# Optimization experiments

Measured on AMD Instinct MI355X. Metric: run time of the kernel, lower is better.

Reference implementation:

```python
import jax, jax.numpy as jnp
import numpy as np

B, L, D, H = 2, 1024, 1024, 16
HD = D // H  # head_dim = 64
EPS = 1e-12  # F.normalize default eps


def setup_inputs() -> dict:
    key = jax.random.key(0)
    ks = jax.random.split(key, 7)
    s = 1.0 / np.sqrt(D)
    return {
        "x": jax.random.normal(ks[0], (B, L, D), dtype=jnp.float32),
        "Wq": jax.random.normal(ks[1], (D, D), dtype=jnp.float32) * s,
        "Wk": jax.random.normal(ks[2], (D, D), dtype=jnp.float32) * s,
        "Wv": jax.random.normal(ks[3], (D, D), dtype=jnp.float32) * s,
        "Wo": jax.random.normal(ks[4], (D, D), dtype=jnp.float32) * s,
        "Wb": jax.random.normal(ks[5], (D, H), dtype=jnp.float32) * s,
        "bb": jnp.zeros((H,), dtype=jnp.float32),
    }


def _l2norm(t):
    # matches F.normalize(t, dim=-1): t / max(||t||_2, eps)
    n = jnp.sqrt(jnp.sum(t * t, axis=-1, keepdims=True))
    return t / jnp.maximum(n, EPS)


def reference(x, Wq, Wk, Wv, Wo, Wb, bb):
    q = (x @ Wq).reshape(B, L, H, HD)
    k = (x @ Wk).reshape(B, L, H, HD)
    v = (x @ Wv).reshape(B, L, H, HD)
    beta = jax.nn.sigmoid(x @ Wb + bb)          # [B, L, H]
    q = _l2norm(q)
    k = _l2norm(k)
    # gated outer products: [B, L, H, HD, HD]
    kv = jnp.einsum('blhd,blhe->blhde', k, v) * beta[..., None, None]
    kv_cumsum = jnp.cumsum(kv, axis=1)          # causal cumulative kv state
    out = jnp.einsum('blhd,blhde->blhe', q, kv_cumsum)  # [B, L, H, HD]
    return out.reshape(B, L, D) @ Wo
```

## Files before the change

kernel.cpp:

```cpp
#include <hip/hip_runtime.h>
#include <math.h>

#define BB   2
#define LL   1024
#define DD   1024
#define HH   16
#define HDIM 64
#define MM   (BB * LL)
#define CHK  64
#define NCHK (LL / CHK)

typedef short bf16x8 __attribute__((ext_vector_type(8)));
typedef float f32x4  __attribute__((ext_vector_type(4)));
typedef const __attribute__((address_space(1))) unsigned int* gas_ptr;
typedef __attribute__((address_space(3))) unsigned int* las_ptr;

__device__ __forceinline__ void gload16(const void* g, void* l) {
    __builtin_amdgcn_global_load_lds((gas_ptr)(unsigned long long)g,
                                     (las_ptr)(unsigned long long)l, 16, 0, 0);
}

__device__ __forceinline__ unsigned short f2bf(float f) {
    unsigned int u = __float_as_uint(f);
    u += 0x7fffu + ((u >> 16) & 1u);
    return (unsigned short)(u >> 16);
}
__device__ __forceinline__ float bfhi(unsigned int u) { return __uint_as_float(u & 0xffff0000u); }
__device__ __forceinline__ float bflo(unsigned int u) { return __uint_as_float(u << 16); }

__device__ __forceinline__ bf16x8 frag70(const unsigned short* a, int row, int tc) {
    const unsigned int* p = (const unsigned int*)(a + row * 70 + tc);
    union { unsigned int u[4]; bf16x8 v; } r;
    r.u[0] = p[0]; r.u[1] = p[1]; r.u[2] = p[2]; r.u[3] = p[3];
    return r.v;
}

__global__ void prep_kernel(const float* __restrict__ x, unsigned short* __restrict__ xb,
                            const float* __restrict__ Wb, float* __restrict__ Wbt) {
    const int bid = blockIdx.x;
    if (bid < 2048) {
        const int idx = bid * 256 + threadIdx.x;
        const float4 v = ((const float4*)x)[idx];
        ushort4 o;
        o.x = f2bf(v.x); o.y = f2bf(v.y); o.z = f2bf(v.z); o.w = f2bf(v.w);
        ((ushort4*)xb)[idx] = o;
    } else {
        const int t = (bid - 2048) * 256 + threadIdx.x;
        const int h = t >> 10, k = t & 1023;
        Wbt[t] = Wb[k * HH + h];
    }
}

__global__ void transpose_cast(const float* __restrict__ W0, const float* __restrict__ W1,
                               const float* __restrict__ W2, const float* __restrict__ W3,
                               unsigned short* __restrict__ T0, unsigned short* __restrict__ T1,
                               unsigned short* __restrict__ T2, unsigned short* __restrict__ T3) {
    __shared__ float tile[32][33];
    const int which = blockIdx.x >> 10;
    const int b = blockIdx.x & 1023;
    const int bk = b >> 5, bn = b & 31;
    const float* W = which == 0 ? W0 : which == 1 ? W1 : which == 2 ? W2 : W3;
    unsigned short* T = which == 0 ? T0 : which == 1 ? T1 : which == 2 ? T2 : T3;
    const int tx = threadIdx.x & 31, ty = threadIdx.x >> 5;
#pragma unroll
    for (int i = 0; i < 4; ++i)
        tile[ty + i * 8][tx] = W[(size_t)(bk * 32 + ty + i * 8) * DD + bn * 32 + tx];
    __syncthreads();
#pragma unroll
    for (int i = 0; i < 4; ++i)
        T[(size_t)(bn * 32 + ty + i * 8) * DD + bk * 32 + tx] = f2bf(tile[tx][ty + i * 8]);
}

__device__ __forceinline__ void gemm_kloop(const unsigned short* A, const unsigned short* Bt,
                                           unsigned short* As, unsigned short* Bs,
                                           int rowBase, int colBase, int K,
                                           f32x4 acc[4][4]) {
    const int tid = threadIdx.x;
    const int c0 = tid, c1 = tid + 256;
    const int ar0 = c0 >> 2, ak0 = (c0 & 3) << 3;
    const int ar1 = c1 >> 2, ak1 = (c1 & 3) << 3;
    const unsigned short* Ag0 = A + (size_t)(rowBase + ar0) * K + ak0;
    const unsigned short* Ag1 = A + (size_t)(rowBase + ar1) * K + ak1;
    const unsigned short* Bg0 = Bt + (size_t)(colBase + ar0) * K + ak0;
    const unsigned short* Bg1 = Bt + (size_t)(colBase + ar1) * K + ak1;
    unsigned short* Al0 = As + c0 * 8; unsigned short* Al1 = As + c1 * 8;
    unsigned short* Bl0 = Bs + c0 * 8; unsigned short* Bl1 = Bs + c1 * 8;
    const int lane = tid & 63, wv = tid >> 6;
    const int qr = wv >> 1, qc = wv & 1;
    const int fr = lane & 15;
    const int koff = (lane >> 4) << 3;
    int aoff[4], boff[4];
#pragma unroll
    for (int mi = 0; mi < 4; ++mi) aoff[mi] = (qr * 64 + mi * 16 + fr) * 32 + koff;
#pragma unroll
    for (int nj = 0; nj < 4; ++nj) boff[nj] = (qc * 64 + nj * 16 + fr) * 32 + koff;

    for (int k0 = 0; k0 < K; k0 += 32) {
        __syncthreads();
        gload16(Ag0, Al0); gload16(Ag1, Al1);
        gload16(Bg0, Bl0); gload16(Bg1, Bl1);
        Ag0 += 32; Ag1 += 32; Bg0 += 32; Bg1 += 32;
        __syncthreads();
        bf16x8 av[4], bv[4];
#pragma unroll
        for (int mi = 0; mi < 4; ++mi) av[mi] = *(const bf16x8*)(As + aoff[mi]);
#pragma unroll
        for (int nj = 0; nj < 4; ++nj) bv[nj] = *(const bf16x8*)(Bs + boff[nj]);
#pragma unroll
        for (int mi = 0; mi < 4; ++mi)
#pragma unroll
            for (int nj = 0; nj < 4; ++nj)
                acc[mi][nj] = __builtin_amdgcn_mfma_f32_16x16x32_bf16(av[mi], bv[nj], acc[mi][nj], 0, 0, 0);
    }
}

__global__ __launch_bounds__(256) void gemm_qkv(const unsigned short* __restrict__ xb,
                                                const unsigned short* __restrict__ Wqt,
                                                const unsigned short* __restrict__ Wkt,
                                                const unsigned short* __restrict__ Wvt,
                                                unsigned short* __restrict__ qb,
                                                unsigned short* __restrict__ kb,
                                                unsigned short* __restrict__ vb) {
    __shared__ unsigned short As[128 * 32];
    __shared__ unsigned short Bs[128 * 32];
    const int by = blockIdx.x / 24, bxx = blockIdx.x % 24;
    const int mat = bxx >> 3, tn = bxx & 7;
    const unsigned short* Bt = mat == 0 ? Wqt : (mat == 1 ? Wkt : Wvt);
    unsigned short* Cout = mat == 0 ? qb : (mat == 1 ? kb : vb);
    f32x4 acc[4][4];
#pragma unroll
    for (int mi = 0; mi < 4; ++mi)
#pragma unroll
        for (int nj = 0; nj < 4; ++nj) acc[mi][nj] = (f32x4){0.f, 0.f, 0.f, 0.f};
    gemm_kloop(xb, Bt, As, Bs, by * 128, tn * 128, DD, acc);

    const int lane = threadIdx.x & 63, wv = threadIdx.x >> 6;
    const int qr = wv >> 1, qc = wv & 1;
    if (mat < 2) {
#pragma unroll
        for (int mi = 0; mi < 4; ++mi)
#pragma unroll
            for (int i = 0; i < 4; ++i) {
                float s = 0.f;
#pragma unroll
                for (int nj = 0; nj < 4; ++nj) { float t = acc[mi][nj][i]; s += t * t; }
                s += __shfl_xor(s, 1, 64);
                s += __shfl_xor(s, 2, 64);
                s += __shfl_xor(s, 4, 64);
                s += __shfl_xor(s, 8, 64);
                const float inv = 1.0f / fmaxf(sqrtf(s), 1e-12f);
#pragma unroll
                for (int nj = 0; nj < 4; ++nj) acc[mi][nj][i] *= inv;
            }
    }
#pragma unroll
    for (int mi = 0; mi < 4; ++mi)
#pragma unroll
        for (int i = 0; i < 4; ++i) {
            const int row = by * 128 + qr * 64 + mi * 16 + (lane >> 4) * 4 + i;
#pragma unroll
            for (int nj = 0; nj < 4; ++nj) {
                const int col = tn * 128 + qc * 64 + nj * 16 + (lane & 15);
                Cout[(size_t)row * DD + col] = f2bf(acc[mi][nj][i]);
            }
        }
}

__global__ __launch_bounds__(256) void gemm_out(const unsigned short* __restrict__ yb,
                                                const unsigned short* __restrict__ Wot,
                                                float* __restrict__ out) {
    __shared__ unsigned short As[64 * 32];
    __shared__ unsigned short Bs[128 * 32];
    const int by = blockIdx.x >> 3, tn = blockIdx.x & 7;
    const int tid = threadIdx.x;
    const int rowBase = by * 64, colBase = tn * 128;
    const int ar = tid >> 2, ak = (tid & 3) << 3;
    const unsigned short* Ag = yb + (size_t)(rowBase + ar) * DD + ak;
    unsigned short* Al = As + tid * 8;
    const int c1 = tid + 256;
    const int br1 = c1 >> 2, bk1 = (c1 & 3) << 3;
    const unsigned short* Bg0 = Wot + (size_t)(colBase + ar) * DD + ak;
    const unsigned short* Bg1 = Wot + (size_t)(colBase + br1) * DD + bk1;
    unsigned short* Bl0 = Bs + tid * 8; unsigned short* Bl1 = Bs + c1 * 8;
    const int lane = tid & 63, wv = tid >> 6;
    const int rh = wv & 1, ch = wv >> 1;
    const int fr = lane & 15, koff = (lane >> 4) << 3;
    int aoff[2], boff[4];
#pragma unroll
    for (int mi = 0; mi < 2; ++mi) aoff[mi] = (rh * 32 + mi * 16 + fr) * 32 + koff;
#pragma unroll
    for (int nj = 0; nj < 4; ++nj) boff[nj] = (ch * 64 + nj * 16 + fr) * 32 + koff;
    f32x4 acc[2][4];
#pragma unroll
    for (int mi = 0; mi < 2; ++mi)
#pragma unroll
        for (int nj = 0; nj < 4; ++nj) acc[mi][nj] = (f32x4){0.f, 0.f, 0.f, 0.f};
    for (int k0 = 0; k0 < DD; k0 += 32) {
        __syncthreads();
        gload16(Ag, Al); gload16(Bg0, Bl0); gload16(Bg1, Bl1);
        Ag += 32; Bg0 += 32; Bg1 += 32;
        __syncthreads();
        bf16x8 av[2], bv[4];
#pragma unroll
        for (int mi = 0; mi < 2; ++mi) av[mi] = *(const bf16x8*)(As + aoff[mi]);
#pragma unroll
        for (int nj = 0; nj < 4; ++nj) bv[nj] = *(const bf16x8*)(Bs + boff[nj]);
#pragma unroll
        for (int mi = 0; mi < 2; ++mi)
#pragma unroll
            for (int nj = 0; nj < 4; ++nj)
                acc[mi][nj] = __builtin_amdgcn_mfma_f32_16x16x32_bf16(av[mi], bv[nj], acc[mi][nj], 0, 0, 0);
    }
    const int quad = lane >> 4;
#pragma unroll
    for (int mi = 0; mi < 2; ++mi)
#pragma unroll
        for (int i = 0; i < 4; ++i) {
            const int row = rowBase + rh * 32 + mi * 16 + quad * 4 + i;
#pragma unroll
            for (int nj = 0; nj < 4; ++nj) {
                const int col = colBase + ch * 64 + nj * 16 + fr;
                out[(size_t)row * DD + col] = acc[mi][nj][i];
            }
        }
}

__global__ void beta_kernel(const float* __restrict__ x, const float* __restrict__ Wbt,
                            const float* __restrict__ bias, float* __restrict__ beta) {
    const int m = blockIdx.x * 4 + (threadIdx.x >> 6);
    const int lane = threadIdx.x & 63;
    const float4* xr = (const float4*)(x + (size_t)m * DD);
    float4 xv[4];
#pragma unroll
    for (int i = 0; i < 4; ++i) xv[i] = xr[lane * 4 + i];
    float res = 0.f;
#pragma unroll
    for (int h = 0; h < HH; ++h) {
        const float4* wr = (const float4*)(Wbt + (size_t)h * DD);
        float s = 0.f;
#pragma unroll
        for (int i = 0; i < 4; ++i) {
            const float4 w = wr[lane * 4 + i];
            s += xv[i].x * w.x + xv[i].y * w.y + xv[i].z * w.z + xv[i].w * w.w;
        }
        s += __shfl_xor(s, 1, 64);  s += __shfl_xor(s, 2, 64);
        s += __shfl_xor(s, 4, 64);  s += __shfl_xor(s, 8, 64);
        s += __shfl_xor(s, 16, 64); s += __shfl_xor(s, 32, 64);
        if (lane == h) res = s;
    }
    if (lane < HH) beta[m * HH + lane] = 1.0f / (1.0f + expf(-(res + bias[lane])));
}

__global__ __launch_bounds__(256) void chunkkv_kernel(const unsigned short* __restrict__ k,
                                                      const unsigned short* __restrict__ v,
                                                      const float* __restrict__ beta,
                                                      float* __restrict__ states) {
    const int c = blockIdx.x % NCHK;
    const int bh = blockIdx.x / NCHK;
    const int b = bh / HH, h = bh % HH;
    __shared__ unsigned short kT[64 * 70];
    __shared__ unsigned short vT[64 * 70];
    const int tid = threadIdx.x;
    for (int i = tid; i < 512; i += 256) {
        const int t = i >> 3, dg = (i & 7) << 3;
        const int m = b * LL + c * CHK + t;
        const float be = beta[m * HH + h];
        const size_t go = (size_t)m * DD + h * 64 + dg;
        const uint4 ku = *(const uint4*)&k[go];
        const uint4 vu = *(const uint4*)&v[go];
        unsigned int kw[4] = {ku.x, ku.y, ku.z, ku.w};
        unsigned int vw[4] = {vu.x, vu.y, vu.z, vu.w};
#pragma unroll
        for (int jj = 0; jj < 4; ++jj) {
            kT[(dg + 2 * jj)     * 70 + t] = f2bf(bflo(kw[jj]) * be);
            kT[(dg + 2 * jj + 1) * 70 + t] = f2bf(bfhi(kw[jj]) * be);
            vT[(dg + 2 * jj)     * 70 + t] = (unsigned short)(vw[jj] & 0xffffu);
            vT[(dg + 2 * jj + 1) * 70 + t] = (unsigned short)(vw[jj] >> 16);
        }
    }
    __syncthreads();
    const int lane = tid & 63, wv = tid >> 6;
    const int fr = lane & 15, quad = lane >> 4;
    f32x4 acc[4];
#pragma unroll
    for (int et = 0; et < 4; ++et) acc[et] = (f32x4){0.f, 0.f, 0.f, 0.f};
#pragma unroll
    for (int kh = 0; kh < 2; ++kh) {
        const int tc = kh * 32 + quad * 8;
        const bf16x8 a = frag70(kT, wv * 16 + fr, tc);
#pragma unroll
        for (int et = 0; et < 4; ++et) {
            const bf16x8 bb = frag70(vT, et * 16 + fr, tc);
            acc[et] = __builtin_amdgcn_mfma_f32_16x16x32_bf16(a, bb, acc[et], 0, 0, 0);
        }
    }
    float* outp = states + ((size_t)bh * NCHK + c) * 4096;
#pragma unroll
    for (int et = 0; et < 4; ++et)
#pragma unroll
        for (int i = 0; i < 4; ++i) {
            const int d = wv * 16 + quad * 4 + i;
            const int e = et * 16 + fr;
            outp[d * 64 + e] = acc[et][i];
        }
}

__global__ void prefix_kernel(float* __restrict__ states) {
    const int bh = blockIdx.x >> 4, pg = blockIdx.x & 15;
    float* base = states + (size_t)bh * NCHK * 4096 + pg * 256 + threadIdx.x;
    float vals[NCHK];
#pragma unroll
    for (int c = 0; c < NCHK; ++c) vals[c] = base[c * 4096];
    float run = 0.0f;
#pragma unroll
    for (int c = 0; c < NCHK; ++c) {
        base[c * 4096] = run;
        run += vals[c];
    }
}

__global__ __launch_bounds__(256) void attn_kernel(const unsigned short* __restrict__ q,
                                                   const unsigned short* __restrict__ k,
                                                   const unsigned short* __restrict__ v,
                                                   const float* __restrict__ beta,
                                                   const float* __restrict__ states,
                                                   unsigned short* __restrict__ y) {
    const int c = blockIdx.x % NCHK;
    const int bh = blockIdx.x / NCHK;
    const int b = bh / HH, h = bh % HH;
    __shared__ unsigned short qS[64 * 80];
    __shared__ unsigned short kS[64 * 80];
    __shared__ unsigned short sS[64 * 80];
    __shared__ unsigned short vT[64 * 70];
    __shared__ unsigned short sT[64 * 70];
    const int tid = threadIdx.x;
    const float* stg = states + ((size_t)bh * NCHK + c) * 4096;
    for (int i = tid; i < 512; i += 256) {
        const int t = i >> 3, dg = (i & 7) << 3;
        const int m = b * LL + c * CHK + t;
        const float be = beta[m * HH + h];
        const size_t go = (size_t)m * DD + h * 64 + dg;
        const uint4 qu = *(const uint4*)&q[go];
        const uint4 ku = *(const uint4*)&k[go];
        const uint4 vu = *(const uint4*)&v[go];
        *(uint4*)&qS[t * 80 + dg] = qu;
        *(uint4*)&kS[t * 80 + dg] = ku;
        unsigned int vw[4] = {vu.x, vu.y, vu.z, vu.w};
#pragma unroll
        for (int jj = 0; jj < 4; ++jj) {
            vT[(dg + 2 * jj)     * 70 + t] = f2bf(bflo(vw[jj]) * be);
            vT[(dg + 2 * jj + 1) * 70 + t] = f2bf(bfhi(vw[jj]) * be);
        }
    }
    for (int i = tid; i < 1024; i += 256) {
        const int d = i >> 4, eg = (i & 15) << 2;
        const float4 s4 = ((const float4*)stg)[i];
        sT[(eg + 0) * 70 + d] = f2bf(s4.x);
        sT[(eg + 1) * 70 + d] = f2bf(s4.y);
        sT[(eg + 2) * 70 + d] = f2bf(s4.z);
        sT[(eg + 3) * 70 + d] = f2bf(s4.w);
    }
    __syncthreads();
    const int lane = tid & 63, wv = tid >> 6;
    const int fr = lane & 15, quad = lane >> 4;
    const int koff = quad * 8;
    f32x4 s_acc[4];
#pragma unroll
    for (int j = 0; j < 4; ++j) s_acc[j] = (f32x4){0.f, 0.f, 0.f, 0.f};
#pragma unroll
    for (int kh = 0; kh < 2; ++kh) {
        const bf16x8 a = *(const bf16x8*)&qS[(wv * 16 + fr) * 80 + kh * 32 + koff];
#pragma unroll
        for (int j = 0; j < 4; ++j) {
            const bf16x8 bb = *(const bf16x8*)&kS[(j * 16 + fr) * 80 + kh * 32 + koff];
            s_acc[j] = __builtin_amdgcn_mfma_f32_16x16x32_bf16(a, bb, s_acc[j], 0, 0, 0);
        }
    }
#pragma unroll
    for (int j = 0; j < 4; ++j)
#pragma unroll
        for (int i = 0; i < 4; ++i) {
            const int t = wv * 16 + quad * 4 + i;
            const int s = j * 16 + fr;
            sS[t * 80 + s] = (s <= t) ? f2bf(s_acc[j][i]) : (unsigned short)0;
        }
    f32x4 o_acc[4];
#pragma unroll
    for (int j = 0; j < 4; ++j) o_acc[j] = (f32x4){0.f, 0.f, 0.f, 0.f};
#pragma unroll
    for (int kh = 0; kh < 2; ++kh) {
        const bf16x8 a = *(const bf16x8*)&sS[(wv * 16 + fr) * 80 + kh * 32 + koff];
#pragma unroll
        for (int j = 0; j < 4; ++j) {
            const bf16x8 bb = frag70(vT, j * 16 + fr, kh * 32 + koff);
            o_acc[j] = __builtin_amdgcn_mfma_f32_16x16x32_bf16(a, bb, o_acc[j], 0, 0, 0);
        }
    }
#pragma unroll
    for (int kh = 0; kh < 2; ++kh) {
        const bf16x8 a = *(const bf16x8*)&qS[(wv * 16 + fr) * 80 + kh * 32 + koff];
#pragma unroll
        for (int j = 0; j < 4; ++j) {
            const bf16x8 bb = frag70(sT, j * 16 + fr, kh * 32 + koff);
            o_acc[j] = __builtin_amdgcn_mfma_f32_16x16x32_bf16(a, bb, o_acc[j], 0, 0, 0);
        }
    }
#pragma unroll
    for (int j = 0; j < 4; ++j)
#pragma unroll
        for (int i = 0; i < 4; ++i) {
            const int m = b * LL + c * CHK + wv * 16 + quad * 4 + i;
            const int e = j * 16 + fr;
            y[(size_t)m * DD + h * 64 + e] = f2bf(o_acc[j][i]);
        }
}

extern "C" void kernel_launch(void* const* d_in, const int* in_sizes, int n_in,
                              void* d_out, int out_size, void* d_ws, size_t ws_size,
                              hipStream_t stream) {
    (void)in_sizes; (void)n_in; (void)out_size; (void)ws_size;
    const float* x  = (const float*)d_in[0];
    const float* Wq = (const float*)d_in[1];
    const float* Wk = (const float*)d_in[2];
    const float* Wv = (const float*)d_in[3];
    const float* Wo = (const float*)d_in[4];
    const float* Wb = (const float*)d_in[5];
    const float* bbp = (const float*)d_in[6];
    float* out = (float*)d_out;

    char* ws = (char*)d_ws;
    unsigned short* xb  = (unsigned short*)ws;                      ws += (size_t)MM * DD * 2;
    unsigned short* Wqt = (unsigned short*)ws;                      ws += (size_t)DD * DD * 2;
    unsigned short* Wkt = (unsigned short*)ws;                      ws += (size_t)DD * DD * 2;
    unsigned short* Wvt = (unsigned short*)ws;                      ws += (size_t)DD * DD * 2;
    unsigned short* Wot = (unsigned short*)ws;                      ws += (size_t)DD * DD * 2;
    float*          Wbt = (float*)ws;                               ws += (size_t)HH * DD * 4;
    unsigned short* qb  = (unsigned short*)ws;                      ws += (size_t)MM * DD * 2;
    unsigned short* kb  = (unsigned short*)ws;                      ws += (size_t)MM * DD * 2;
    unsigned short* vb  = (unsigned short*)ws;                      ws += (size_t)MM * DD * 2;
    unsigned short* yb  = (unsigned short*)ws;                      ws += (size_t)MM * DD * 2;
    float*          beta   = (float*)ws;                            ws += (size_t)MM * HH * 4;
    float*          states = (float*)ws;                            ws += (size_t)BB * HH * NCHK * 4096 * 4;

    prep_kernel<<<2112, 256, 0, stream>>>(x, xb, Wb, Wbt);
    transpose_cast<<<4096, 256, 0, stream>>>(Wq, Wk, Wv, Wo, Wqt, Wkt, Wvt, Wot);
    gemm_qkv<<<16 * 24, 256, 0, stream>>>(xb, Wqt, Wkt, Wvt, qb, kb, vb);
    beta_kernel<<<MM / 4, 256, 0, stream>>>(x, Wbt, bbp, beta);
    chunkkv_kernel<<<BB * HH * NCHK, 256, 0, stream>>>(kb, vb, beta, states);
    prefix_kernel<<<BB * HH * NCHK, 256, 0, stream>>>(states);
    attn_kernel<<<BB * HH * NCHK, 256, 0, stream>>>(qb, kb, vb, beta, states, yb);
    gemm_out<<<32 * 8, 256, 0, stream>>>(yb, Wot, out);
}
```

Baseline: 155.3 us.

## Fuse prep kernels, compute beta via MFMA in QKV GEMM, sequential chunk scan

Merges the input-cast and weight-transpose kernels into one launch, moves the beta projection into extra blocks of the QKV GEMM using bf16 MFMA, and replaces the three-kernel chunked state pipeline (chunk kv, prefix, attention) with one scan kernel per batch-head. The scan keeps the running state in registers, so the global state buffer and two launches go away. The cost is that the scan runs only 32 blocks, each walking 16 chunks serially, which leaves most CUs idle. Beta now uses bf16 inputs, which lowers its precision.

```diff
diff --git a/kernel.cpp b/kernel.cpp
--- a/kernel.cpp
+++ b/kernel.cpp
@@ -35,8 +35,12 @@
     return r.v;
 }
 
-__global__ void prep_kernel(const float* __restrict__ x, unsigned short* __restrict__ xb,
-                            const float* __restrict__ Wb, float* __restrict__ Wbt) {
+__global__ void prep_all(const float* __restrict__ x, unsigned short* __restrict__ xb,
+                         const float* __restrict__ Wb, unsigned short* __restrict__ Wbt,
+                         const float* __restrict__ W0, const float* __restrict__ W1,
+                         const float* __restrict__ W2, const float* __restrict__ W3,
+                         unsigned short* __restrict__ T0, unsigned short* __restrict__ T1,
+                         unsigned short* __restrict__ T2, unsigned short* __restrict__ T3) {
     const int bid = blockIdx.x;
     if (bid < 2048) {
         const int idx = bid * 256 + threadIdx.x;
@@ -44,20 +48,18 @@
         ushort4 o;
         o.x = f2bf(v.x); o.y = f2bf(v.y); o.z = f2bf(v.z); o.w = f2bf(v.w);
         ((ushort4*)xb)[idx] = o;
-    } else {
+        return;
+    }
+    if (bid < 2112) {
         const int t = (bid - 2048) * 256 + threadIdx.x;
-        const int h = t >> 10, k = t & 1023;
-        Wbt[t] = Wb[k * HH + h];
-    }
-}
-
-__global__ void transpose_cast(const float* __restrict__ W0, const float* __restrict__ W1,
-                               const float* __restrict__ W2, const float* __restrict__ W3,
-                               unsigned short* __restrict__ T0, unsigned short* __restrict__ T1,
-                               unsigned short* __restrict__ T2, unsigned short* __restrict__ T3) {
+        const int h = t >> 10, kidx = t & 1023;
+        Wbt[t] = f2bf(Wb[kidx * HH + h]);
+        return;
+    }
     __shared__ float tile[32][33];
-    const int which = blockIdx.x >> 10;
-    const int b = blockIdx.x & 1023;
+    const int b4 = bid - 2112;
+    const int which = b4 >> 10;
+    const int b = b4 & 1023;
     const int bk = b >> 5, bn = b & 31;
     const float* W = which == 0 ? W0 : which == 1 ? W1 : which == 2 ? W2 : W3;
     unsigned short* T = which == 0 ? T0 : which == 1 ? T1 : which == 2 ? T2 : T3;
@@ -114,15 +116,45 @@
     }
 }
 
-__global__ __launch_bounds__(256) void gemm_qkv(const unsigned short* __restrict__ xb,
-                                                const unsigned short* __restrict__ Wqt,
-                                                const unsigned short* __restrict__ Wkt,
-                                                const unsigned short* __restrict__ Wvt,
-                                                unsigned short* __restrict__ qb,
-                                                unsigned short* __restrict__ kb,
-                                                unsigned short* __restrict__ vb) {
+__global__ __launch_bounds__(256) void gemm_qkv_beta(const unsigned short* __restrict__ xb,
+                                                     const unsigned short* __restrict__ Wqt,
+                                                     const unsigned short* __restrict__ Wkt,
+                                                     const unsigned short* __restrict__ Wvt,
+                                                     const unsigned short* __restrict__ Wbt,
+                                                     const float* __restrict__ bbp,
+                                                     unsigned short* __restrict__ qb,
+                                                     unsigned short* __restrict__ kb,
+                                                     unsigned short* __restrict__ vb,
+                                                     float* __restrict__ beta) {
     __shared__ unsigned short As[128 * 32];
     __shared__ unsigned short Bs[128 * 32];
+    const int lane = threadIdx.x & 63, wv = threadIdx.x >> 6;
+    const int fr = lane & 15, quad = lane >> 4;
+    if (blockIdx.x >= 384) {
+        const int rowBase = (blockIdx.x - 384) * 128;
+        const int r0 = rowBase + wv * 32 + fr;
+        f32x4 bacc[2];
+        bacc[0] = (f32x4){0.f, 0.f, 0.f, 0.f};
+        bacc[1] = (f32x4){0.f, 0.f, 0.f, 0.f};
+        for (int k0 = 0; k0 < DD; k0 += 32) {
+            const int kk = k0 + quad * 8;
+            const bf16x8 a0 = *(const bf16x8*)&xb[(size_t)r0 * DD + kk];
+            const bf16x8 a1 = *(const bf16x8*)&xb[(size_t)(r0 + 16) * DD + kk];
+            const bf16x8 bw = *(const bf16x8*)&Wbt[(size_t)fr * DD + kk];
+            bacc[0] = __builtin_amdgcn_mfma_f32_16x16x32_bf16(a0, bw, bacc[0], 0, 0, 0);
+            bacc[1] = __builtin_amdgcn_mfma_f32_16x16x32_bf16(a1, bw, bacc[1], 0, 0, 0);
+        }
+        const float bias = bbp[fr];
+#pragma unroll
+        for (int mi = 0; mi < 2; ++mi)
+#pragma unroll
+            for (int i = 0; i < 4; ++i) {
+                const int row = rowBase + wv * 32 + mi * 16 + quad * 4 + i;
+                const float s = bacc[mi][i] + bias;
+                beta[row * HH + fr] = 1.0f / (1.0f + expf(-s));
+            }
+        return;
+    }
     const int by = blockIdx.x / 24, bxx = blockIdx.x % 24;
     const int mat = bxx >> 3, tn = bxx & 7;
     const unsigned short* Bt = mat == 0 ? Wqt : (mat == 1 ? Wkt : Wvt);
@@ -134,7 +166,6 @@
         for (int nj = 0; nj < 4; ++nj) acc[mi][nj] = (f32x4){0.f, 0.f, 0.f, 0.f};
     gemm_kloop(xb, Bt, As, Bs, by * 128, tn * 128, DD, acc);
 
-    const int lane = threadIdx.x & 63, wv = threadIdx.x >> 6;
     const int qr = wv >> 1, qc = wv & 1;
     if (mat < 2) {
 #pragma unroll
@@ -157,13 +188,122 @@
     for (int mi = 0; mi < 4; ++mi)
 #pragma unroll
         for (int i = 0; i < 4; ++i) {
-            const int row = by * 128 + qr * 64 + mi * 16 + (lane >> 4) * 4 + i;
+            const int row = by * 128 + qr * 64 + mi * 16 + quad * 4 + i;
 #pragma unroll
             for (int nj = 0; nj < 4; ++nj) {
-                const int col = tn * 128 + qc * 64 + nj * 16 + (lane & 15);
+                const int col = tn * 128 + qc * 64 + nj * 16 + fr;
                 Cout[(size_t)row * DD + col] = f2bf(acc[mi][nj][i]);
             }
         }
+}
+
+__global__ __launch_bounds__(256) void scan_kernel(const unsigned short* __restrict__ q,
+                                                   const unsigned short* __restrict__ k,
+                                                   const unsigned short* __restrict__ v,
+                                                   const float* __restrict__ beta,
+                                                   unsigned short* __restrict__ y) {
+    const int bh = blockIdx.x;
+    const int b = bh >> 4, h = bh & 15;
+    __shared__ unsigned short qS[64 * 80];
+    __shared__ unsigned short kS[64 * 80];
+    __shared__ unsigned short pS[64 * 80];
+    __shared__ unsigned short kT[64 * 70];
+    __shared__ unsigned short vT[64 * 70];
+    __shared__ unsigned short sT[64 * 70];
+    const int tid = threadIdx.x;
+    const int lane = tid & 63, wv = tid >> 6;
+    const int fr = lane & 15, quad = lane >> 4;
+    f32x4 st[4];
+#pragma unroll
+    for (int et = 0; et < 4; ++et) st[et] = (f32x4){0.f, 0.f, 0.f, 0.f};
+
+    for (int c = 0; c < NCHK; ++c) {
+        __syncthreads();
+#pragma unroll
+        for (int et = 0; et < 4; ++et)
+#pragma unroll
+            for (int i = 0; i < 4; ++i)
+                sT[(et * 16 + fr) * 70 + wv * 16 + quad * 4 + i] = f2bf(st[et][i]);
+#pragma unroll
+        for (int i2 = tid; i2 < 512; i2 += 256) {
+            const int t = i2 >> 3, dg = (i2 & 7) << 3;
+            const int m = b * LL + c * CHK + t;
+            const float be = beta[m * HH + h];
+            const size_t go = (size_t)m * DD + h * 64 + dg;
+            const uint4 qu = *(const uint4*)&q[go];
+            const uint4 ku = *(const uint4*)&k[go];
+            const uint4 vu = *(const uint4*)&v[go];
+            *(uint4*)&qS[t * 80 + dg] = qu;
+            *(uint4*)&kS[t * 80 + dg] = ku;
+            const unsigned int kw[4] = {ku.x, ku.y, ku.z, ku.w};
+            const unsigned int vw[4] = {vu.x, vu.y, vu.z, vu.w};
+#pragma unroll
+            for (int jj = 0; jj < 4; ++jj) {
+                kT[(dg + 2 * jj)     * 70 + t] = (unsigned short)(kw[jj] & 0xffffu);
+                kT[(dg + 2 * jj + 1) * 70 + t] = (unsigned short)(kw[jj] >> 16);
+                vT[(dg + 2 * jj)     * 70 + t] = f2bf(bflo(vw[jj]) * be);
+                vT[(dg + 2 * jj + 1) * 70 + t] = f2bf(bfhi(vw[jj]) * be);
+            }
+        }
+        __syncthreads();
+        f32x4 sacc[4];
+#pragma unroll
+        for (int j = 0; j < 4; ++j) sacc[j] = (f32x4){0.f, 0.f, 0.f, 0.f};
+#pragma unroll
+        for (int kh = 0; kh < 2; ++kh) {
+            const bf16x8 a = *(const bf16x8*)&qS[(wv * 16 + fr) * 80 + kh * 32 + quad * 8];
+#pragma unroll
+            for (int j = 0; j < 4; ++j) {
+                const bf16x8 bbf = *(const bf16x8*)&kS[(j * 16 + fr) * 80 + kh * 32 + quad * 8];
+                sacc[j] = __builtin_amdgcn_mfma_f32_16x16x32_bf16(a, bbf, sacc[j], 0, 0, 0);
+            }
+        }
+#pragma unroll
+        for (int j = 0; j < 4; ++j)
+#pragma unroll
+            for (int i = 0; i < 4; ++i) {
+                const int t = wv * 16 + quad * 4 + i;
+                const int s = j * 16 + fr;
+                pS[t * 80 + s] = (s <= t) ? f2bf(sacc[j][i]) : (unsigned short)0;
+            }
+        f32x4 oacc[4];
+#pragma unroll
+        for (int j = 0; j < 4; ++j) oacc[j] = (f32x4){0.f, 0.f, 0.f, 0.f};
+#pragma unroll
+        for (int kh = 0; kh < 2; ++kh) {
+            const bf16x8 a = *(const bf16x8*)&pS[(wv * 16 + fr) * 80 + kh * 32 + quad * 8];
+#pragma unroll
+            for (int j = 0; j < 4; ++j) {
+                const bf16x8 bbf = frag70(vT, j * 16 + fr, kh * 32 + quad * 8);
+                oacc[j] = __builtin_amdgcn_mfma_f32_16x16x32_bf16(a, bbf, oacc[j], 0, 0, 0);
+            }
+        }
+#pragma unroll
+        for (int kh = 0; kh < 2; ++kh) {
+            const bf16x8 a = *(const bf16x8*)&qS[(wv * 16 + fr) * 80 + kh * 32 + quad * 8];
+#pragma unroll
+            for (int j = 0; j < 4; ++j) {
+                const bf16x8 bbf = frag70(sT, j * 16 + fr, kh * 32 + quad * 8);
+                oacc[j] = __builtin_amdgcn_mfma_f32_16x16x32_bf16(a, bbf, oacc[j], 0, 0, 0);
+            }
+        }
+#pragma unroll
+        for (int j = 0; j < 4; ++j)
+#pragma unroll
+            for (int i = 0; i < 4; ++i) {
+                const int m = b * LL + c * CHK + wv * 16 + quad * 4 + i;
+                y[(size_t)m * DD + h * 64 + j * 16 + fr] = f2bf(oacc[j][i]);
+            }
+#pragma unroll
+        for (int kh = 0; kh < 2; ++kh) {
+            const bf16x8 a = frag70(kT, wv * 16 + fr, kh * 32 + quad * 8);
+#pragma unroll
+            for (int et = 0; et < 4; ++et) {
+                const bf16x8 bbf = frag70(vT, et * 16 + fr, kh * 32 + quad * 8);
+                st[et] = __builtin_amdgcn_mfma_f32_16x16x32_bf16(a, bbf, st[et], 0, 0, 0);
+            }
+        }
+    }
 }
 
 __global__ __launch_bounds__(256) void gemm_out(const unsigned short* __restrict__ yb,
@@ -225,196 +365,6 @@
         }
 }
 
-__global__ void beta_kernel(const float* __restrict__ x, const float* __restrict__ Wbt,
-                            const float* __restrict__ bias, float* __restrict__ beta) {
-    const int m = blockIdx.x * 4 + (threadIdx.x >> 6);
-    const int lane = threadIdx.x & 63;
-    const float4* xr = (const float4*)(x + (size_t)m * DD);
-    float4 xv[4];
-#pragma unroll
-    for (int i = 0; i < 4; ++i) xv[i] = xr[lane * 4 + i];
-    float res = 0.f;
-#pragma unroll
-    for (int h = 0; h < HH; ++h) {
-        const float4* wr = (const float4*)(Wbt + (size_t)h * DD);
-        float s = 0.f;
-#pragma unroll
-        for (int i = 0; i < 4; ++i) {
-            const float4 w = wr[lane * 4 + i];
-            s += xv[i].x * w.x + xv[i].y * w.y + xv[i].z * w.z + xv[i].w * w.w;
-        }
-        s += __shfl_xor(s, 1, 64);  s += __shfl_xor(s, 2, 64);
-        s += __shfl_xor(s, 4, 64);  s += __shfl_xor(s, 8, 64);
-        s += __shfl_xor(s, 16, 64); s += __shfl_xor(s, 32, 64);
-        if (lane == h) res = s;
-    }
-    if (lane < HH) beta[m * HH + lane] = 1.0f / (1.0f + expf(-(res + bias[lane])));
-}
-
-__global__ __launch_bounds__(256) void chunkkv_kernel(const unsigned short* __restrict__ k,
-                                                      const unsigned short* __restrict__ v,
-                                                      const float* __restrict__ beta,
-                                                      float* __restrict__ states) {
-    const int c = blockIdx.x % NCHK;
-    const int bh = blockIdx.x / NCHK;
-    const int b = bh / HH, h = bh % HH;
-    __shared__ unsigned short kT[64 * 70];
-    __shared__ unsigned short vT[64 * 70];
-    const int tid = threadIdx.x;
-    for (int i = tid; i < 512; i += 256) {
-        const int t = i >> 3, dg = (i & 7) << 3;
-        const int m = b * LL + c * CHK + t;
-        const float be = beta[m * HH + h];
-        const size_t go = (size_t)m * DD + h * 64 + dg;
-        const uint4 ku = *(const uint4*)&k[go];
-        const uint4 vu = *(const uint4*)&v[go];
-        unsigned int kw[4] = {ku.x, ku.y, ku.z, ku.w};
-        unsigned int vw[4] = {vu.x, vu.y, vu.z, vu.w};
-#pragma unroll
-        for (int jj = 0; jj < 4; ++jj) {
-            kT[(dg + 2 * jj)     * 70 + t] = f2bf(bflo(kw[jj]) * be);
-            kT[(dg + 2 * jj + 1) * 70 + t] = f2bf(bfhi(kw[jj]) * be);
-            vT[(dg + 2 * jj)     * 70 + t] = (unsigned short)(vw[jj] & 0xffffu);
-            vT[(dg + 2 * jj + 1) * 70 + t] = (unsigned short)(vw[jj] >> 16);
-        }
-    }
-    __syncthreads();
-    const int lane = tid & 63, wv = tid >> 6;
-    const int fr = lane & 15, quad = lane >> 4;
-    f32x4 acc[4];
-#pragma unroll
-    for (int et = 0; et < 4; ++et) acc[et] = (f32x4){0.f, 0.f, 0.f, 0.f};
-#pragma unroll
-    for (int kh = 0; kh < 2; ++kh) {
-        const int tc = kh * 32 + quad * 8;
-        const bf16x8 a = frag70(kT, wv * 16 + fr, tc);
-#pragma unroll
-        for (int et = 0; et < 4; ++et) {
-            const bf16x8 bb = frag70(vT, et * 16 + fr, tc);
-            acc[et] = __builtin_amdgcn_mfma_f32_16x16x32_bf16(a, bb, acc[et], 0, 0, 0);
-        }
-    }
-    float* outp = states + ((size_t)bh * NCHK + c) * 4096;
-#pragma unroll
-    for (int et = 0; et < 4; ++et)
-#pragma unroll
-        for (int i = 0; i < 4; ++i) {
-            const int d = wv * 16 + quad * 4 + i;
-            const int e = et * 16 + fr;
-            outp[d * 64 + e] = acc[et][i];
-        }
-}
-
-__global__ void prefix_kernel(float* __restrict__ states) {
-    const int bh = blockIdx.x >> 4, pg = blockIdx.x & 15;
-    float* base = states + (size_t)bh * NCHK * 4096 + pg * 256 + threadIdx.x;
-    float vals[NCHK];
-#pragma unroll
-    for (int c = 0; c < NCHK; ++c) vals[c] = base[c * 4096];
-    float run = 0.0f;
-#pragma unroll
-    for (int c = 0; c < NCHK; ++c) {
-        base[c * 4096] = run;
-        run += vals[c];
-    }
-}
-
-__global__ __launch_bounds__(256) void attn_kernel(const unsigned short* __restrict__ q,
-                                                   const unsigned short* __restrict__ k,
-                                                   const unsigned short* __restrict__ v,
-                                                   const float* __restrict__ beta,
-                                                   const float* __restrict__ states,
-                                                   unsigned short* __restrict__ y) {
-    const int c = blockIdx.x % NCHK;
-    const int bh = blockIdx.x / NCHK;
-    const int b = bh / HH, h = bh % HH;
-    __shared__ unsigned short qS[64 * 80];
-    __shared__ unsigned short kS[64 * 80];
-    __shared__ unsigned short sS[64 * 80];
-    __shared__ unsigned short vT[64 * 70];
-    __shared__ unsigned short sT[64 * 70];
-    const int tid = threadIdx.x;
-    const float* stg = states + ((size_t)bh * NCHK + c) * 4096;
-    for (int i = tid; i < 512; i += 256) {
-        const int t = i >> 3, dg = (i & 7) << 3;
-        const int m = b * LL + c * CHK + t;
-        const float be = beta[m * HH + h];
-        const size_t go = (size_t)m * DD + h * 64 + dg;
-        const uint4 qu = *(const uint4*)&q[go];
-        const uint4 ku = *(const uint4*)&k[go];
-        const uint4 vu = *(const uint4*)&v[go];
-        *(uint4*)&qS[t * 80 + dg] = qu;
-        *(uint4*)&kS[t * 80 + dg] = ku;
-        unsigned int vw[4] = {vu.x, vu.y, vu.z, vu.w};
-#pragma unroll
-        for (int jj = 0; jj < 4; ++jj) {
-            vT[(dg + 2 * jj)     * 70 + t] = f2bf(bflo(vw[jj]) * be);
-            vT[(dg + 2 * jj + 1) * 70 + t] = f2bf(bfhi(vw[jj]) * be);
-        }
-    }
-    for (int i = tid; i < 1024; i += 256) {
-        const int d = i >> 4, eg = (i & 15) << 2;
-        const float4 s4 = ((const float4*)stg)[i];
-        sT[(eg + 0) * 70 + d] = f2bf(s4.x);
-        sT[(eg + 1) * 70 + d] = f2bf(s4.y);
-        sT[(eg + 2) * 70 + d] = f2bf(s4.z);
-        sT[(eg + 3) * 70 + d] = f2bf(s4.w);
-    }
-    __syncthreads();
-    const int lane = tid & 63, wv = tid >> 6;
-    const int fr = lane & 15, quad = lane >> 4;
-    const int koff = quad * 8;
-    f32x4 s_acc[4];
-#pragma unroll
-    for (int j = 0; j < 4; ++j) s_acc[j] = (f32x4){0.f, 0.f, 0.f, 0.f};
-#pragma unroll
-    for (int kh = 0; kh < 2; ++kh) {
-        const bf16x8 a = *(const bf16x8*)&qS[(wv * 16 + fr) * 80 + kh * 32 + koff];
-#pragma unroll
-        for (int j = 0; j < 4; ++j) {
-            const bf16x8 bb = *(const bf16x8*)&kS[(j * 16 + fr) * 80 + kh * 32 + koff];
-            s_acc[j] = __builtin_amdgcn_mfma_f32_16x16x32_bf16(a, bb, s_acc[j], 0, 0, 0);
-        }
-    }
-#pragma unroll
-    for (int j = 0; j < 4; ++j)
-#pragma unroll
-        for (int i = 0; i < 4; ++i) {
-            const int t = wv * 16 + quad * 4 + i;
-            const int s = j * 16 + fr;
-            sS[t * 80 + s] = (s <= t) ? f2bf(s_acc[j][i]) : (unsigned short)0;
-        }
-    f32x4 o_acc[4];
-#pragma unroll
-    for (int j = 0; j < 4; ++j) o_acc[j] = (f32x4){0.f, 0.f, 0.f, 0.f};
-#pragma unroll
-    for (int kh = 0; kh < 2; ++kh) {
-        const bf16x8 a = *(const bf16x8*)&sS[(wv * 16 + fr) * 80 + kh * 32 + koff];
-#pragma unroll
-        for (int j = 0; j < 4; ++j) {
-            const bf16x8 bb = frag70(vT, j * 16 + fr, kh * 32 + koff);
-            o_acc[j] = __builtin_amdgcn_mfma_f32_16x16x32_bf16(a, bb, o_acc[j], 0, 0, 0);
-        }
-    }
-#pragma unroll
-    for (int kh = 0; kh < 2; ++kh) {
-        const bf16x8 a = *(const bf16x8*)&qS[(wv * 16 + fr) * 80 + kh * 32 + koff];
-#pragma unroll
-        for (int j = 0; j < 4; ++j) {
-            const bf16x8 bb = frag70(sT, j * 16 + fr, kh * 32 + koff);
-            o_acc[j] = __builtin_amdgcn_mfma_f32_16x16x32_bf16(a, bb, o_acc[j], 0, 0, 0);
-        }
-    }
-#pragma unroll
-    for (int j = 0; j < 4; ++j)
-#pragma unroll
-        for (int i = 0; i < 4; ++i) {
-            const int m = b * LL + c * CHK + wv * 16 + quad * 4 + i;
-            const int e = j * 16 + fr;
-            y[(size_t)m * DD + h * 64 + e] = f2bf(o_acc[j][i]);
-        }
-}
-
 extern "C" void kernel_launch(void* const* d_in, const int* in_sizes, int n_in,
                               void* d_out, int out_size, void* d_ws, size_t ws_size,
                               hipStream_t stream) {
@@ -434,20 +384,15 @@
     unsigned short* Wkt = (unsigned short*)ws;                      ws += (size_t)DD * DD * 2;
     unsigned short* Wvt = (unsigned short*)ws;                      ws += (size_t)DD * DD * 2;
     unsigned short* Wot = (unsigned short*)ws;                      ws += (size_t)DD * DD * 2;
-    float*          Wbt = (float*)ws;                               ws += (size_t)HH * DD * 4;
+    unsigned short* Wbt = (unsigned short*)ws;                      ws += (size_t)HH * DD * 2;
     unsigned short* qb  = (unsigned short*)ws;                      ws += (size_t)MM * DD * 2;
     unsigned short* kb  = (unsigned short*)ws;                      ws += (size_t)MM * DD * 2;
     unsigned short* vb  = (unsigned short*)ws;                      ws += (size_t)MM * DD * 2;
     unsigned short* yb  = (unsigned short*)ws;                      ws += (size_t)MM * DD * 2;
     float*          beta   = (float*)ws;                            ws += (size_t)MM * HH * 4;
-    float*          states = (float*)ws;                            ws += (size_t)BB * HH * NCHK * 4096 * 4;
-
-    prep_kernel<<<2112, 256, 0, stream>>>(x, xb, Wb, Wbt);
-    transpose_cast<<<4096, 256, 0, stream>>>(Wq, Wk, Wv, Wo, Wqt, Wkt, Wvt, Wot);
-    gemm_qkv<<<16 * 24, 256, 0, stream>>>(xb, Wqt, Wkt, Wvt, qb, kb, vb);
-    beta_kernel<<<MM / 4, 256, 0, stream>>>(x, Wbt, bbp, beta);
-    chunkkv_kernel<<<BB * HH * NCHK, 256, 0, stream>>>(kb, vb, beta, states);
-    prefix_kernel<<<BB * HH * NCHK, 256, 0, stream>>>(states);
-    attn_kernel<<<BB * HH * NCHK, 256, 0, stream>>>(qb, kb, vb, beta, states, yb);
+
+    prep_all<<<6208, 256, 0, stream>>>(x, xb, Wb, Wbt, Wq, Wk, Wv, Wo, Wqt, Wkt, Wvt, Wot);
+    gemm_qkv_beta<<<400, 256, 0, stream>>>(xb, Wqt, Wkt, Wvt, Wbt, bbp, qb, kb, vb, beta);
+    scan_kernel<<<BB * HH, 256, 0, stream>>>(qb, kb, vb, beta, yb);
     gemm_out<<<32 * 8, 256, 0, stream>>>(yb, Wot, out);
 }
```

Result: slower. 174.0 us (+12.0%).
